# Kernel optimization log

Hardware: AMD Instinct MI355X
Metric: run time of the kernel (lower is better)

Reference implementation:

```python
import jax, jax.numpy as jnp
import numpy as np

B, N, F_IN, H, C = 256, 512, 14, 30, 2
CLUSTERS = [8, 4, 2, 1]


def _gcn(x, adj, W, b):
    # DenseGCNConv: set diagonal of adj to 1 (self loops), sym-normalize, propagate
    n = adj.shape[-1]
    eye = jnp.eye(n, dtype=adj.dtype)
    a = adj * (1.0 - eye) + eye
    dis = jnp.clip(a.sum(-1), 1.0, None) ** -0.5  # [B, n]
    a = dis[..., :, None] * a * dis[..., None, :]
    return jnp.einsum('bij,bjh->bih', a, x @ W) + b


def _diff_pool(x, adj, W, b):
    # DiffPool module applies softmax over node dim (dim=1), then
    # dense_diff_pool applies softmax over cluster dim (dim=-1)
    s = jax.nn.softmax(x @ W + b, axis=1)
    s = jax.nn.softmax(s, axis=-1)          # [B, n, c]
    xp = jnp.einsum('bnc,bnf->bcf', s, x)
    ap = jnp.einsum('bnc,bnm,bmd->bcd', s, adj, s)
    link = jnp.linalg.norm(adj - jnp.einsum('bnc,bmc->bnm', s, s)) / adj.size
    ent = jnp.mean(jnp.sum(-s * jnp.log(s + 1e-15), axis=-1))
    return xp, ap, link, ent


def _forward(x, adj, cws, cbs, pws, pbs, lw, lb):
    r = jax.nn.relu
    x = r(_gcn(x, adj, cws[0], cbs[0]))
    x = r(_gcn(x, adj, cws[1], cbs[1]))
    x = r(_gcn(x, adj, cws[2], cbs[2]))
    x = _gcn(x, adj, cws[3], cbs[3])        # no relu before first pool
    x, adj, _, _ = _diff_pool(x, adj, pws[0], pbs[0])
    x = r(_gcn(x, adj, cws[4], cbs[4]))
    x, adj, _, _ = _diff_pool(x, adj, pws[1], pbs[1])
    x = r(_gcn(x, adj, cws[5], cbs[5]))
    x, adj, _, _ = _diff_pool(x, adj, pws[2], pbs[2])
    x = r(_gcn(x, adj, cws[6], cbs[6]))
    x, adj, _, _ = _diff_pool(x, adj, pws[3], pbs[3])
    x = r(_gcn(x, adj, cws[7], cbs[7]))     # [B, 1, H]
    return (x @ lw + lb).squeeze()          # [B, C]


def setup_inputs() -> dict:
    key = jax.random.key(0)
    ks = jax.random.split(key, 40)
    inp = {}
    inp['x'] = jax.random.normal(ks[0], (B, N, F_IN), jnp.float32)
    inp['adj'] = (jax.random.uniform(ks[1], (B, N, N)) < 0.05).astype(jnp.float32)
    inp['edge_index'] = jax.random.randint(ks[2], (2, 4096), 0, N, dtype=jnp.int32)
    inp['batch'] = jnp.zeros((B * N,), jnp.int32)
    dims = [(F_IN, H)] + [(H, H)] * 7
    for i, (di, do) in enumerate(dims):
        inp[f'cw{i}'] = jax.random.normal(ks[3 + i], (di, do), jnp.float32) * (di ** -0.5)
        inp[f'cb{i}'] = jnp.zeros((do,), jnp.float32)
    for i, c in enumerate(CLUSTERS):
        inp[f'pw{i}'] = jax.random.normal(ks[12 + i], (H, c), jnp.float32) * (H ** -0.5)
        inp[f'pb{i}'] = jnp.zeros((c,), jnp.float32)
    inp['lw'] = jax.random.normal(ks[20], (H, C), jnp.float32) * (H ** -0.5)
    inp['lb'] = jnp.zeros((C,), jnp.float32)
    return inp


def reference(x, adj, edge_index, batch,
              cw0, cb0, cw1, cb1, cw2, cb2, cw3, cb3,
              cw4, cb4, cw5, cb5, cw6, cb6, cw7, cb7,
              pw0, pb0, pw1, pb1, pw2, pb2, pw3, pb3,
              lw, lb):
    cws = [cw0, cw1, cw2, cw3, cw4, cw5, cw6, cw7]
    cbs = [cb0, cb1, cb2, cb3, cb4, cb5, cb6, cb7]
    pws = [pw0, pw1, pw2, pw3]
    pbs = [pb0, pb1, pb2, pb3]
    return _forward(x, adj, cws, cbs, pws, pbs, lw, lb)
```

## Files before the change

kernel.cpp:

```cpp
#include <hip/hip_runtime.h>
#include <cstdint>
#include <cstddef>

#define B_ 256
#define N_ 512
#define RCAP 72
#define STRX 36

typedef unsigned short u16;

constexpr size_t O_COLIDX = 0;
constexpr size_t O_ROWCNT = 18874368;
constexpr size_t O_DIS    = 19398656;
constexpr size_t O_DIAG   = 19922944;

__global__ __launch_bounds__(256) void build_sparse(
    const float* __restrict__ adj, u16* __restrict__ colidx,
    int* __restrict__ rowcnt, float* __restrict__ dis, float* __restrict__ diagv)
{
    int row  = blockIdx.x * 4 + (threadIdx.x >> 6);
    int lane = threadIdx.x & 63;
    int i    = row & (N_ - 1);
    const float4* arow = (const float4*)(adj + (size_t)row * N_);
    float4 v0 = arow[lane];
    float4 v1 = arow[lane + 64];
    float vals[8] = {v0.x, v0.y, v0.z, v0.w, v1.x, v1.y, v1.z, v1.w};

    float sum = 0.f, dloc = 0.f;
    int cnt = 0;
    #pragma unroll
    for (int k = 0; k < 8; ++k) {
        int jc = (k < 4) ? (lane * 4 + k) : (256 + lane * 4 + (k - 4));
        float v = vals[k];
        if (jc == i) dloc = v;
        else { sum += v; if (v != 0.f) ++cnt; }
    }
    int pre = cnt;
    #pragma unroll
    for (int d = 1; d < 64; d <<= 1) { int y = __shfl_up(pre, d, 64); if (lane >= d) pre += y; }
    int excl  = pre - cnt;
    int total = __shfl(pre, 63, 64);
    #pragma unroll
    for (int d = 32; d > 0; d >>= 1) { sum += __shfl_xor(sum, d, 64); dloc += __shfl_xor(dloc, d, 64); }

    u16* cb = colidx + (size_t)row * RCAP;
    int c2 = 0;
    #pragma unroll
    for (int k = 0; k < 8; ++k) {
        int jc = (k < 4) ? (lane * 4 + k) : (256 + lane * 4 + (k - 4));
        float v = vals[k];
        if (jc != i && v != 0.f) { int p = excl + c2; if (p < RCAP) cb[p] = (u16)jc; ++c2; }
    }
    int base = total > RCAP ? RCAP : total;
    int p1 = base + lane;      if (p1 < RCAP) cb[p1] = (u16)N_;
    int p2 = base + 64 + lane; if (p2 < RCAP) cb[p2] = (u16)N_;
    if (lane == 0) {
        rowcnt[row] = (base + 7) >> 3;
        dis[row]    = rsqrtf(fmaxf(1.f, sum + 1.f));
        diagv[row]  = dloc;
    }
}

template <int FIN, bool RELU>
__device__ __forceinline__ void gcn_layer(
    int t, float di, int nch, const u16* __restrict__ CIDX, float* __restrict__ XA,
    const float* __restrict__ Wg, const float* __restrict__ bg, float* xr)
{
    float acc[32];
    #pragma unroll
    for (int h = 0; h < 32; ++h) acc[h] = 0.f;
    #pragma unroll
    for (int f = 0; f < FIN; ++f) {
        float xv = xr[f];
        #pragma unroll
        for (int h = 0; h < 30; ++h) acc[h] = fmaf(xv, Wg[f * 30 + h], acc[h]);
    }
    #pragma unroll
    for (int h = 0; h < 30; ++h) acc[h] *= di;
    #pragma unroll
    for (int d = 0; d < 8; ++d)
        *(float4*)&XA[t * STRX + 4 * d] =
            make_float4(acc[4*d], acc[4*d+1], acc[4*d+2], acc[4*d+3]);
    __syncthreads();

    for (int ch = 0; ch < nch; ++ch) {
        uint4 cw = *(const uint4*)&CIDX[t * RCAP + ch * 8];
        int j0 = (int)(cw.x & 0xffffu), j1 = (int)(cw.x >> 16);
        int j2 = (int)(cw.y & 0xffffu), j3 = (int)(cw.y >> 16);
        int j4 = (int)(cw.z & 0xffffu), j5 = (int)(cw.z >> 16);
        int j6 = (int)(cw.w & 0xffffu), j7 = (int)(cw.w >> 16);
        #define ACCROW(JJ) { const float* rp = &XA[(JJ) * STRX]; \
            _Pragma("unroll") for (int d = 0; d < 8; ++d) { \
                const float4 v = *(const float4*)&rp[4 * d]; \
                acc[4*d+0] += v.x; acc[4*d+1] += v.y; \
                acc[4*d+2] += v.z; acc[4*d+3] += v.w; } }
        ACCROW(j0) ACCROW(j1) ACCROW(j2) ACCROW(j3)
        ACCROW(j4) ACCROW(j5) ACCROW(j6) ACCROW(j7)
        #undef ACCROW
    }
    #pragma unroll
    for (int h = 0; h < 30; ++h) {
        float r = fmaf(di, acc[h], bg[h]);
        if (RELU) r = fmaxf(r, 0.f);
        xr[h] = r;
    }
    __syncthreads();
}

__device__ void gcn_small(int n, int t, const float* X, float* XN, float* XW, float* DIS,
                          const float* A, const float* W, const float* Bias, bool relu)
{
    if (t < n) {
        float s = 1.f;
        for (int jj = 0; jj < n; ++jj) if (jj != t) s += A[t * 8 + jj];
        DIS[t] = rsqrtf(fmaxf(1.f, s));
    }
    __syncthreads();
    if (t < n * 30) {
        int i = t / 30, h = t - i * 30;
        float acc = 0.f;
        #pragma unroll
        for (int f = 0; f < 30; ++f) acc += X[i * 30 + f] * W[f * 30 + h];
        XW[t] = acc * DIS[i];
    }
    __syncthreads();
    if (t < n * 30) {
        int i = t / 30, h = t - i * 30;
        float acc = XW[i * 30 + h];
        for (int jj = 0; jj < n; ++jj) if (jj != i) acc += A[i * 8 + jj] * XW[jj * 30 + h];
        float r = DIS[i] * acc + Bias[h];
        if (relu) r = fmaxf(r, 0.f);
        XN[t] = r;
    }
    __syncthreads();
}

__device__ void pool_small(int n, int c, int t, const float* X, const float* A,
                           const float* PW, const float* PB,
                           float* S, float* T, float* LG, float* XN, float* AN)
{
    if (t < n * c) {
        int i = t / c, k = t - i * c;
        float acc = PB[k];
        #pragma unroll
        for (int h = 0; h < 30; ++h) acc += X[i * 30 + h] * PW[h * c + k];
        LG[i * 8 + k] = acc;
    }
    __syncthreads();
    if (t < c) {
        float mx = -1e30f;
        for (int i = 0; i < n; ++i) mx = fmaxf(mx, LG[i * 8 + t]);
        float sm = 0.f;
        for (int i = 0; i < n; ++i) { float e = __expf(LG[i * 8 + t] - mx); LG[i * 8 + t] = e; sm += e; }
        float inv = 1.f / sm;
        for (int i = 0; i < n; ++i) LG[i * 8 + t] *= inv;
    }
    __syncthreads();
    if (t < n) {
        float mx = -1e30f;
        for (int k = 0; k < c; ++k) mx = fmaxf(mx, LG[t * 8 + k]);
        float sm = 0.f;
        for (int k = 0; k < c; ++k) { float e = __expf(LG[t * 8 + k] - mx); S[t * 8 + k] = e; sm += e; }
        float inv = 1.f / sm;
        for (int k = 0; k < c; ++k) S[t * 8 + k] *= inv;
    }
    __syncthreads();
    if (t < c * 30) {
        int k = t / 30, f = t - k * 30;
        float acc = 0.f;
        for (int i = 0; i < n; ++i) acc += S[i * 8 + k] * X[i * 30 + f];
        XN[t] = acc;
    }
    if (t < n * c) {
        int i = t / c, d = t - i * c;
        float acc = 0.f;
        for (int m = 0; m < n; ++m) acc += A[i * 8 + m] * S[m * 8 + d];
        T[i * 8 + d] = acc;
    }
    __syncthreads();
    if (t < c * c) {
        int k = t / c, d = t - k * c;
        float acc = 0.f;
        for (int i = 0; i < n; ++i) acc += S[i * 8 + k] * T[i * 8 + d];
        AN[k * 8 + d] = acc;
    }
    __syncthreads();
}

__global__ __launch_bounds__(512) void mega2_kernel(
    const float* __restrict__ x0,
    const float* __restrict__ W0, const float* __restrict__ Bs0,
    const float* __restrict__ W1, const float* __restrict__ Bs1,
    const float* __restrict__ W2, const float* __restrict__ Bs2,
    const float* __restrict__ W3, const float* __restrict__ Bs3,
    const float* __restrict__ pw, const float* __restrict__ pb,
    const float* cw4, const float* cb4, const float* cw5, const float* cb5,
    const float* cw6, const float* cb6, const float* cw7, const float* cb7,
    const float* pw1, const float* pb1, const float* pw2, const float* pb2,
    const float* pw3, const float* pb3, const float* lw, const float* lb,
    const u16* __restrict__ colidx, const int* __restrict__ rowcnt,
    const float* __restrict__ dis, const float* __restrict__ diagv,
    float* __restrict__ out)
{
    __shared__ __align__(16) u16   CIDX[N_ * RCAP];
    __shared__ __align__(16) float XA[(N_ + 1) * STRX];
    __shared__ float bufX[240], bufY[240], TXW[240], TDIS[8];
    __shared__ float bufA[64], bufB[64], TS[64], TT[64], TLG[64];

    const int b = blockIdx.x, t = threadIdx.x;

    {
        const unsigned* g32 = (const unsigned*)(colidx + (size_t)b * N_ * RCAP);
        unsigned* l32 = (unsigned*)CIDX;
        #pragma unroll
        for (int i = 0; i < N_ * RCAP / 2; i += 512) l32[i + t] = g32[i + t];
    }
    int   nch = rowcnt[(size_t)b * N_ + t];
    float di  = dis  [(size_t)b * N_ + t];
    float dg  = diagv[(size_t)b * N_ + t];

    if (t < STRX) XA[N_ * STRX + t] = 0.f;

    float xr[30];
    {
        const float2* xrow = (const float2*)(x0 + ((size_t)b * N_ + t) * 14);
        #pragma unroll
        for (int k = 0; k < 7; ++k) { float2 v = xrow[k]; xr[2*k] = v.x; xr[2*k+1] = v.y; }
    }
    __syncthreads();

    gcn_layer<14, true >(t, di, nch, CIDX, XA, W0, Bs0, xr);
    gcn_layer<30, true >(t, di, nch, CIDX, XA, W1, Bs1, xr);
    gcn_layer<30, true >(t, di, nch, CIDX, XA, W2, Bs2, xr);
    gcn_layer<30, false>(t, di, nch, CIDX, XA, W3, Bs3, xr);

    float* ls   = XA;
    float* ltp  = XA + 6156;
    float* red  = XA + 12300;
    float* red2 = XA + 14348;
    float* X3   = (float*)CIDX;

    {
        float lg[8];
        #pragma unroll
        for (int c = 0; c < 8; ++c) lg[c] = pb[c];
        #pragma unroll
        for (int h = 0; h < 30; ++h) {
            float xv = xr[h];
            #pragma unroll
            for (int c = 0; c < 8; ++c) lg[c] = fmaf(xv, pw[h * 8 + c], lg[c]);
        }
        *(float4*)&ls[t * 12]     = make_float4(lg[0], lg[1], lg[2], lg[3]);
        *(float4*)&ls[t * 12 + 4] = make_float4(lg[4], lg[5], lg[6], lg[7]);
        if (t < 8) ls[N_ * 12 + t] = 0.f;
    }
    __syncthreads();
    {
        int c = t >> 6, lane = t & 63;
        float v[8]; float mx = -1e30f;
        #pragma unroll
        for (int k = 0; k < 8; ++k) { v[k] = ls[(k * 64 + lane) * 12 + c]; mx = fmaxf(mx, v[k]); }
        #pragma unroll
        for (int d = 32; d > 0; d >>= 1) mx = fmaxf(mx, __shfl_xor(mx, d, 64));
        float sm = 0.f;
        #pragma unroll
        for (int k = 0; k < 8; ++k) { v[k] = __expf(v[k] - mx); sm += v[k]; }
        #pragma unroll
        for (int d = 32; d > 0; d >>= 1) sm += __shfl_xor(sm, d, 64);
        float inv = 1.f / sm;
        #pragma unroll
        for (int k = 0; k < 8; ++k) ls[(k * 64 + lane) * 12 + c] = v[k] * inv;
    }
    __syncthreads();
    float s8[8];
    {
        float mx = -1e30f;
        #pragma unroll
        for (int c = 0; c < 8; ++c) { s8[c] = ls[t * 12 + c]; mx = fmaxf(mx, s8[c]); }
        float sm = 0.f;
        #pragma unroll
        for (int c = 0; c < 8; ++c) { s8[c] = __expf(s8[c] - mx); sm += s8[c]; }
        float inv = 1.f / sm;
        #pragma unroll
        for (int c = 0; c < 8; ++c) s8[c] *= inv;
        *(float4*)&ls[t * 12]     = make_float4(s8[0], s8[1], s8[2], s8[3]);
        *(float4*)&ls[t * 12 + 4] = make_float4(s8[4], s8[5], s8[6], s8[7]);
    }
    __syncthreads();
    {
        float a8[8];
        #pragma unroll
        for (int d = 0; d < 8; ++d) a8[d] = dg * s8[d];
        for (int ch = 0; ch < nch; ++ch) {
            uint4 cw = *(const uint4*)&CIDX[t * RCAP + ch * 8];
            #define LTROW(JJ) { const float4 u0 = *(const float4*)&ls[(JJ) * 12]; \
                                const float4 u1 = *(const float4*)&ls[(JJ) * 12 + 4]; \
                                a8[0]+=u0.x; a8[1]+=u0.y; a8[2]+=u0.z; a8[3]+=u0.w; \
                                a8[4]+=u1.x; a8[5]+=u1.y; a8[6]+=u1.z; a8[7]+=u1.w; }
            LTROW((int)(cw.x & 0xffffu)) LTROW((int)(cw.x >> 16))
            LTROW((int)(cw.y & 0xffffu)) LTROW((int)(cw.y >> 16))
            LTROW((int)(cw.z & 0xffffu)) LTROW((int)(cw.z >> 16))
            LTROW((int)(cw.w & 0xffffu)) LTROW((int)(cw.w >> 16))
            #undef LTROW
        }
        __syncthreads();
        *(float4*)&ltp[t * 12]     = make_float4(a8[0], a8[1], a8[2], a8[3]);
        *(float4*)&ltp[t * 12 + 4] = make_float4(a8[4], a8[5], a8[6], a8[7]);
    }
    #pragma unroll
    for (int d = 0; d < 7; ++d)
        *(float4*)&X3[t * STRX + 4 * d] =
            make_float4(xr[4*d], xr[4*d+1], xr[4*d+2], xr[4*d+3]);
    *(float4*)&X3[t * STRX + 28] = make_float4(xr[28], xr[29], 0.f, 0.f);
    __syncthreads();
    {
        int seg = t >> 6, cd = t & 63, c = cd >> 3, dd = cd & 7;
        float a0 = 0.f, a1 = 0.f, a2 = 0.f, a3 = 0.f;
        for (int n = seg * 64; n < seg * 64 + 64; ++n) {
            float sv = ls[n * 12 + c];
            const float4 xv = *(const float4*)&X3[n * STRX + 4 * dd];
            a0 = fmaf(sv, xv.x, a0); a1 = fmaf(sv, xv.y, a1);
            a2 = fmaf(sv, xv.z, a2); a3 = fmaf(sv, xv.w, a3);
        }
        *(float4*)&red[t * 4] = make_float4(a0, a1, a2, a3);
    }
    {
        int seg = t >> 6, c = (t >> 3) & 7, d = t & 7;
        float s1 = 0.f;
        for (int n = seg * 64; n < seg * 64 + 64; ++n)
            s1 = fmaf(ls[n * 12 + c], ltp[n * 12 + d], s1);
        red2[t] = s1;
    }
    __syncthreads();
    if (t < 240) {
        int c = t / 30, f = t - c * 30, dd = f >> 2, m = f & 3;
        float s1 = 0.f;
        #pragma unroll
        for (int seg = 0; seg < 8; ++seg) s1 += red[(seg * 64 + c * 8 + dd) * 4 + m];
        bufX[t] = s1;
    }
    if (t < 64) {
        float s1 = 0.f;
        #pragma unroll
        for (int k = 0; k < 8; ++k) s1 += red2[k * 64 + t];
        bufA[t] = s1;
    }
    __syncthreads();

    float *X = bufX, *XN = bufY, *A = bufA, *AN = bufB;
    gcn_small(8, t, X, XN, TXW, TDIS, A, cw4, cb4, true);    { float* tm = X; X = XN; XN = tm; }
    pool_small(8, 4, t, X, A, pw1, pb1, TS, TT, TLG, XN, AN); { float* tm = X; X = XN; XN = tm; tm = A; A = AN; AN = tm; }
    gcn_small(4, t, X, XN, TXW, TDIS, A, cw5, cb5, true);    { float* tm = X; X = XN; XN = tm; }
    pool_small(4, 2, t, X, A, pw2, pb2, TS, TT, TLG, XN, AN); { float* tm = X; X = XN; XN = tm; tm = A; A = AN; AN = tm; }
    gcn_small(2, t, X, XN, TXW, TDIS, A, cw6, cb6, true);    { float* tm = X; X = XN; XN = tm; }
    pool_small(2, 1, t, X, A, pw3, pb3, TS, TT, TLG, XN, AN); { float* tm = X; X = XN; XN = tm; tm = A; A = AN; AN = tm; }
    gcn_small(1, t, X, XN, TXW, TDIS, A, cw7, cb7, true);    { float* tm = X; X = XN; XN = tm; }

    if (t < 2) {
        float acc = lb[t];
        #pragma unroll
        for (int h = 0; h < 30; ++h) acc += X[h] * lw[h * 2 + t];
        out[(size_t)b * 2 + t] = acc;
    }
}

extern "C" void kernel_launch(void* const* d_in, const int* in_sizes, int n_in,
                              void* d_out, int out_size, void* d_ws, size_t ws_size,
                              hipStream_t stream)
{
    const float* x   = (const float*)d_in[0];
    const float* adj = (const float*)d_in[1];
    const float *cw[8], *cb[8], *pw[4], *pb[4];
    for (int i = 0; i < 8; ++i) { cw[i] = (const float*)d_in[4 + 2 * i]; cb[i] = (const float*)d_in[5 + 2 * i]; }
    for (int i = 0; i < 4; ++i) { pw[i] = (const float*)d_in[20 + 2 * i]; pb[i] = (const float*)d_in[21 + 2 * i]; }
    const float* lw = (const float*)d_in[28];
    const float* lb = (const float*)d_in[29];

    char* ws = (char*)d_ws;
    u16*   colidx = (u16*)(ws + O_COLIDX);
    int*   rowcnt = (int*)(ws + O_ROWCNT);
    float* dis0   = (float*)(ws + O_DIS);
    float* diag0  = (float*)(ws + O_DIAG);

    build_sparse<<<(B_ * N_) / 4, 256, 0, stream>>>(adj, colidx, rowcnt, dis0, diag0);
    mega2_kernel<<<B_, 512, 0, stream>>>(x,
        cw[0], cb[0], cw[1], cb[1], cw[2], cb[2], cw[3], cb[3],
        pw[0], pb[0],
        cw[4], cb[4], cw[5], cb[5], cw[6], cb[6], cw[7], cb[7],
        pw[1], pb[1], pw[2], pb[2], pw[3], pb[3], lw, lb,
        colidx, rowcnt, dis0, diag0, (float*)d_out);
}
```

Measured before the change: 173.7 us.

## Split GCN feature dimension across two thread halves with 1024-thread blocks

Doubles the block to 1024 threads so each node is handled by two threads, each owning half of the 30 hidden features (16 and 14). This halves per-thread accumulation registers and work in the sparse aggregation and the pooling phases. Because the shared-memory scratch for the final node features no longer fits, those features are spilled to a global workspace buffer and read back for the pooled-feature reduction. The cost is extra barriers and exchanges to rebuild full rows between layers, plus the global round trip.

```diff
diff --git a/kernel.cpp b/kernel.cpp
--- a/kernel.cpp
+++ b/kernel.cpp
@@ -13,6 +13,7 @@
 constexpr size_t O_ROWCNT = 18874368;
 constexpr size_t O_DIS    = 19398656;
 constexpr size_t O_DIAG   = 19922944;
+constexpr size_t O_X3G    = 20447232;
 
 __global__ __launch_bounds__(256) void build_sparse(
     const float* __restrict__ adj, u16* __restrict__ colidx,
@@ -62,35 +63,46 @@
 }
 
 template <int FIN, bool RELU>
-__device__ __forceinline__ void gcn_layer(
-    int t, float di, int nch, const u16* __restrict__ CIDX, float* __restrict__ XA,
-    const float* __restrict__ Wg, const float* __restrict__ bg, float* xr)
-{
-    float acc[32];
-    #pragma unroll
-    for (int h = 0; h < 32; ++h) acc[h] = 0.f;
-    #pragma unroll
-    for (int f = 0; f < FIN; ++f) {
-        float xv = xr[f];
-        #pragma unroll
-        for (int h = 0; h < 30; ++h) acc[h] = fmaf(xv, Wg[f * 30 + h], acc[h]);
-    }
-    #pragma unroll
-    for (int h = 0; h < 30; ++h) acc[h] *= di;
-    #pragma unroll
-    for (int d = 0; d < 8; ++d)
-        *(float4*)&XA[t * STRX + 4 * d] =
+__device__ __forceinline__ void glayer(
+    int n, int hf, float di, int nch, const u16* __restrict__ CIDX,
+    float* __restrict__ XA, const float* __restrict__ W,
+    const float* __restrict__ Bs, float* xr)
+{
+    float acc[16];
+    #pragma unroll
+    for (int h = 0; h < 16; ++h) acc[h] = 0.f;
+    if (hf == 0) {
+        #pragma unroll
+        for (int f = 0; f < FIN; ++f) {
+            float xv = xr[f];
+            #pragma unroll
+            for (int h = 0; h < 16; ++h) acc[h] = fmaf(xv, W[f * 30 + h], acc[h]);
+        }
+    } else {
+        #pragma unroll
+        for (int f = 0; f < FIN; ++f) {
+            float xv = xr[f];
+            #pragma unroll
+            for (int h = 0; h < 14; ++h) acc[h] = fmaf(xv, W[f * 30 + 16 + h], acc[h]);
+        }
+    }
+    #pragma unroll
+    for (int h = 0; h < 16; ++h) acc[h] *= di;
+    int ho = hf * 16;
+    #pragma unroll
+    for (int d = 0; d < 4; ++d)
+        *(float4*)&XA[n * STRX + ho + 4 * d] =
             make_float4(acc[4*d], acc[4*d+1], acc[4*d+2], acc[4*d+3]);
     __syncthreads();
 
     for (int ch = 0; ch < nch; ++ch) {
-        uint4 cw = *(const uint4*)&CIDX[t * RCAP + ch * 8];
+        uint4 cw = *(const uint4*)&CIDX[n * RCAP + ch * 8];
         int j0 = (int)(cw.x & 0xffffu), j1 = (int)(cw.x >> 16);
         int j2 = (int)(cw.y & 0xffffu), j3 = (int)(cw.y >> 16);
         int j4 = (int)(cw.z & 0xffffu), j5 = (int)(cw.z >> 16);
         int j6 = (int)(cw.w & 0xffffu), j7 = (int)(cw.w >> 16);
-        #define ACCROW(JJ) { const float* rp = &XA[(JJ) * STRX]; \
-            _Pragma("unroll") for (int d = 0; d < 8; ++d) { \
+        #define ACCROW(JJ) { const float* rp = &XA[(JJ) * STRX + ho]; \
+            _Pragma("unroll") for (int d = 0; d < 4; ++d) { \
                 const float4 v = *(const float4*)&rp[4 * d]; \
                 acc[4*d+0] += v.x; acc[4*d+1] += v.y; \
                 acc[4*d+2] += v.z; acc[4*d+3] += v.w; } }
@@ -98,11 +110,44 @@
         ACCROW(j4) ACCROW(j5) ACCROW(j6) ACCROW(j7)
         #undef ACCROW
     }
-    #pragma unroll
-    for (int h = 0; h < 30; ++h) {
-        float r = fmaf(di, acc[h], bg[h]);
-        if (RELU) r = fmaxf(r, 0.f);
-        xr[h] = r;
+    float rr[16];
+    if (hf == 0) {
+        #pragma unroll
+        for (int h = 0; h < 16; ++h) {
+            float r = fmaf(di, acc[h], Bs[h]);
+            rr[h] = RELU ? fmaxf(r, 0.f) : r;
+        }
+    } else {
+        #pragma unroll
+        for (int h = 0; h < 14; ++h) {
+            float r = fmaf(di, acc[h], Bs[16 + h]);
+            rr[h] = RELU ? fmaxf(r, 0.f) : r;
+        }
+        rr[14] = 0.f; rr[15] = 0.f;
+    }
+    __syncthreads();
+    #pragma unroll
+    for (int d = 0; d < 4; ++d)
+        *(float4*)&XA[n * STRX + ho + 4 * d] =
+            make_float4(rr[4*d], rr[4*d+1], rr[4*d+2], rr[4*d+3]);
+    __syncthreads();
+    if (hf == 0) {
+        #pragma unroll
+        for (int h = 0; h < 16; ++h) xr[h] = rr[h];
+        #pragma unroll
+        for (int d = 0; d < 4; ++d) {
+            const float4 v = *(const float4*)&XA[n * STRX + 16 + 4 * d];
+            if (d < 3) { xr[16+4*d] = v.x; xr[17+4*d] = v.y; xr[18+4*d] = v.z; xr[19+4*d] = v.w; }
+            else       { xr[28] = v.x; xr[29] = v.y; }
+        }
+    } else {
+        #pragma unroll
+        for (int h = 0; h < 14; ++h) xr[16 + h] = rr[h];
+        #pragma unroll
+        for (int d = 0; d < 4; ++d) {
+            const float4 v = *(const float4*)&XA[n * STRX + 4 * d];
+            xr[4*d] = v.x; xr[4*d+1] = v.y; xr[4*d+2] = v.z; xr[4*d+3] = v.w;
+        }
     }
     __syncthreads();
 }
@@ -187,7 +232,7 @@
     __syncthreads();
 }
 
-__global__ __launch_bounds__(512) void mega2_kernel(
+__global__ __launch_bounds__(1024) void mega3_kernel(
     const float* __restrict__ x0,
     const float* __restrict__ W0, const float* __restrict__ Bs0,
     const float* __restrict__ W1, const float* __restrict__ Bs1,
@@ -200,7 +245,7 @@
     const float* pw3, const float* pb3, const float* lw, const float* lb,
     const u16* __restrict__ colidx, const int* __restrict__ rowcnt,
     const float* __restrict__ dis, const float* __restrict__ diagv,
-    float* __restrict__ out)
+    float* __restrict__ x3g, float* __restrict__ out)
 {
     __shared__ __align__(16) u16   CIDX[N_ * RCAP];
     __shared__ __align__(16) float XA[(N_ + 1) * STRX];
@@ -208,54 +253,64 @@
     __shared__ float bufA[64], bufB[64], TS[64], TT[64], TLG[64];
 
     const int b = blockIdx.x, t = threadIdx.x;
+    const int n = t & (N_ - 1), hf = t >> 9;
 
     {
         const unsigned* g32 = (const unsigned*)(colidx + (size_t)b * N_ * RCAP);
         unsigned* l32 = (unsigned*)CIDX;
         #pragma unroll
-        for (int i = 0; i < N_ * RCAP / 2; i += 512) l32[i + t] = g32[i + t];
-    }
-    int   nch = rowcnt[(size_t)b * N_ + t];
-    float di  = dis  [(size_t)b * N_ + t];
-    float dg  = diagv[(size_t)b * N_ + t];
-
+        for (int i = 0; i < N_ * RCAP / 2; i += 1024) l32[i + t] = g32[i + t];
+    }
+    int   nch = rowcnt[(size_t)b * N_ + n];
+    float di  = dis  [(size_t)b * N_ + n];
+    float dg  = diagv[(size_t)b * N_ + n];
     if (t < STRX) XA[N_ * STRX + t] = 0.f;
 
     float xr[30];
     {
-        const float2* xrow = (const float2*)(x0 + ((size_t)b * N_ + t) * 14);
+        const float2* xrow = (const float2*)(x0 + ((size_t)b * N_ + n) * 14);
         #pragma unroll
         for (int k = 0; k < 7; ++k) { float2 v = xrow[k]; xr[2*k] = v.x; xr[2*k+1] = v.y; }
     }
     __syncthreads();
 
-    gcn_layer<14, true >(t, di, nch, CIDX, XA, W0, Bs0, xr);
-    gcn_layer<30, true >(t, di, nch, CIDX, XA, W1, Bs1, xr);
-    gcn_layer<30, true >(t, di, nch, CIDX, XA, W2, Bs2, xr);
-    gcn_layer<30, false>(t, di, nch, CIDX, XA, W3, Bs3, xr);
+    glayer<14, true >(n, hf, di, nch, CIDX, XA, W0, Bs0, xr);
+    glayer<30, true >(n, hf, di, nch, CIDX, XA, W1, Bs1, xr);
+    glayer<30, true >(n, hf, di, nch, CIDX, XA, W2, Bs2, xr);
+    glayer<30, false>(n, hf, di, nch, CIDX, XA, W3, Bs3, xr);
+
+    {
+        float4* xgw = (float4*)(x3g + (size_t)b * N_ * 32);
+        #pragma unroll
+        for (int i = 0; i < 4; ++i) {
+            int e4 = t + i * 1024;
+            int nn = e4 >> 3, q = e4 & 7;
+            xgw[e4] = *(const float4*)&XA[nn * STRX + 4 * q];
+        }
+    }
+    float lg[4];
+    {
+        int c0 = hf * 4;
+        #pragma unroll
+        for (int c = 0; c < 4; ++c) lg[c] = pb[c0 + c];
+        #pragma unroll
+        for (int h = 0; h < 30; ++h) {
+            float xv = xr[h];
+            #pragma unroll
+            for (int c = 0; c < 4; ++c) lg[c] = fmaf(xv, pw[h * 8 + c0 + c], lg[c]);
+        }
+    }
+    __syncthreads();
 
     float* ls   = XA;
     float* ltp  = XA + 6156;
     float* red  = XA + 12300;
-    float* red2 = XA + 14348;
-    float* X3   = (float*)CIDX;
-
-    {
-        float lg[8];
-        #pragma unroll
-        for (int c = 0; c < 8; ++c) lg[c] = pb[c];
-        #pragma unroll
-        for (int h = 0; h < 30; ++h) {
-            float xv = xr[h];
-            #pragma unroll
-            for (int c = 0; c < 8; ++c) lg[c] = fmaf(xv, pw[h * 8 + c], lg[c]);
-        }
-        *(float4*)&ls[t * 12]     = make_float4(lg[0], lg[1], lg[2], lg[3]);
-        *(float4*)&ls[t * 12 + 4] = make_float4(lg[4], lg[5], lg[6], lg[7]);
-        if (t < 8) ls[N_ * 12 + t] = 0.f;
-    }
-    __syncthreads();
-    {
+    float* red2 = XA + 16396;
+
+    *(float4*)&ls[n * 12 + hf * 4] = make_float4(lg[0], lg[1], lg[2], lg[3]);
+    if (t < 12) ls[N_ * 12 + t] = 0.f;
+    __syncthreads();
+    if (t < 512) {
         int c = t >> 6, lane = t & 63;
         float v[8]; float mx = -1e30f;
         #pragma unroll
@@ -272,53 +327,42 @@
         for (int k = 0; k < 8; ++k) ls[(k * 64 + lane) * 12 + c] = v[k] * inv;
     }
     __syncthreads();
-    float s8[8];
-    {
-        float mx = -1e30f;
-        #pragma unroll
-        for (int c = 0; c < 8; ++c) { s8[c] = ls[t * 12 + c]; mx = fmaxf(mx, s8[c]); }
+    if (t < 512) {
+        float v[8]; float mx = -1e30f;
+        #pragma unroll
+        for (int c = 0; c < 8; ++c) { v[c] = ls[t * 12 + c]; mx = fmaxf(mx, v[c]); }
         float sm = 0.f;
         #pragma unroll
-        for (int c = 0; c < 8; ++c) { s8[c] = __expf(s8[c] - mx); sm += s8[c]; }
+        for (int c = 0; c < 8; ++c) { v[c] = __expf(v[c] - mx); sm += v[c]; }
         float inv = 1.f / sm;
-        #pragma unroll
-        for (int c = 0; c < 8; ++c) s8[c] *= inv;
-        *(float4*)&ls[t * 12]     = make_float4(s8[0], s8[1], s8[2], s8[3]);
-        *(float4*)&ls[t * 12 + 4] = make_float4(s8[4], s8[5], s8[6], s8[7]);
-    }
-    __syncthreads();
-    {
-        float a8[8];
-        #pragma unroll
-        for (int d = 0; d < 8; ++d) a8[d] = dg * s8[d];
+        *(float4*)&ls[t * 12]     = make_float4(v[0]*inv, v[1]*inv, v[2]*inv, v[3]*inv);
+        *(float4*)&ls[t * 12 + 4] = make_float4(v[4]*inv, v[5]*inv, v[6]*inv, v[7]*inv);
+    }
+    __syncthreads();
+    {
+        int d0 = hf * 4;
+        const float4 sown = *(const float4*)&ls[n * 12 + d0];
+        float a0 = dg * sown.x, a1 = dg * sown.y, a2 = dg * sown.z, a3 = dg * sown.w;
         for (int ch = 0; ch < nch; ++ch) {
-            uint4 cw = *(const uint4*)&CIDX[t * RCAP + ch * 8];
-            #define LTROW(JJ) { const float4 u0 = *(const float4*)&ls[(JJ) * 12]; \
-                                const float4 u1 = *(const float4*)&ls[(JJ) * 12 + 4]; \
-                                a8[0]+=u0.x; a8[1]+=u0.y; a8[2]+=u0.z; a8[3]+=u0.w; \
-                                a8[4]+=u1.x; a8[5]+=u1.y; a8[6]+=u1.z; a8[7]+=u1.w; }
+            uint4 cw = *(const uint4*)&CIDX[n * RCAP + ch * 8];
+            #define LTROW(JJ) { const float4 u0 = *(const float4*)&ls[(JJ) * 12 + d0]; \
+                                a0 += u0.x; a1 += u0.y; a2 += u0.z; a3 += u0.w; }
             LTROW((int)(cw.x & 0xffffu)) LTROW((int)(cw.x >> 16))
             LTROW((int)(cw.y & 0xffffu)) LTROW((int)(cw.y >> 16))
             LTROW((int)(cw.z & 0xffffu)) LTROW((int)(cw.z >> 16))
             LTROW((int)(cw.w & 0xffffu)) LTROW((int)(cw.w >> 16))
             #undef LTROW
         }
-        __syncthreads();
-        *(float4*)&ltp[t * 12]     = make_float4(a8[0], a8[1], a8[2], a8[3]);
-        *(float4*)&ltp[t * 12 + 4] = make_float4(a8[4], a8[5], a8[6], a8[7]);
-    }
-    #pragma unroll
-    for (int d = 0; d < 7; ++d)
-        *(float4*)&X3[t * STRX + 4 * d] =
-            make_float4(xr[4*d], xr[4*d+1], xr[4*d+2], xr[4*d+3]);
-    *(float4*)&X3[t * STRX + 28] = make_float4(xr[28], xr[29], 0.f, 0.f);
+        *(float4*)&ltp[n * 12 + d0] = make_float4(a0, a1, a2, a3);
+    }
     __syncthreads();
     {
         int seg = t >> 6, cd = t & 63, c = cd >> 3, dd = cd & 7;
+        const float4* xg = (const float4*)(x3g + (size_t)b * N_ * 32);
         float a0 = 0.f, a1 = 0.f, a2 = 0.f, a3 = 0.f;
-        for (int n = seg * 64; n < seg * 64 + 64; ++n) {
-            float sv = ls[n * 12 + c];
-            const float4 xv = *(const float4*)&X3[n * STRX + 4 * dd];
+        for (int nn = seg * 32; nn < seg * 32 + 32; ++nn) {
+            float sv = ls[nn * 12 + c];
+            const float4 xv = xg[nn * 8 + dd];
             a0 = fmaf(sv, xv.x, a0); a1 = fmaf(sv, xv.y, a1);
             a2 = fmaf(sv, xv.z, a2); a3 = fmaf(sv, xv.w, a3);
         }
@@ -327,8 +371,8 @@
     {
         int seg = t >> 6, c = (t >> 3) & 7, d = t & 7;
         float s1 = 0.f;
-        for (int n = seg * 64; n < seg * 64 + 64; ++n)
-            s1 = fmaf(ls[n * 12 + c], ltp[n * 12 + d], s1);
+        for (int nn = seg * 32; nn < seg * 32 + 32; ++nn)
+            s1 = fmaf(ls[nn * 12 + c], ltp[nn * 12 + d], s1);
         red2[t] = s1;
     }
     __syncthreads();
@@ -336,14 +380,14 @@
         int c = t / 30, f = t - c * 30, dd = f >> 2, m = f & 3;
         float s1 = 0.f;
         #pragma unroll
-        for (int seg = 0; seg < 8; ++seg) s1 += red[(seg * 64 + c * 8 + dd) * 4 + m];
+        for (int seg = 0; seg < 16; ++seg) s1 += red[(seg * 64 + c * 8 + dd) * 4 + m];
         bufX[t] = s1;
-    }
-    if (t < 64) {
+    } else if (t >= 256 && t < 320) {
+        int tt = t - 256;
         float s1 = 0.f;
         #pragma unroll
-        for (int k = 0; k < 8; ++k) s1 += red2[k * 64 + t];
-        bufA[t] = s1;
+        for (int seg = 0; seg < 16; ++seg) s1 += red2[seg * 64 + tt];
+        bufA[tt] = s1;
     }
     __syncthreads();
 
@@ -381,12 +425,13 @@
     int*   rowcnt = (int*)(ws + O_ROWCNT);
     float* dis0   = (float*)(ws + O_DIS);
     float* diag0  = (float*)(ws + O_DIAG);
+    float* x3g    = (float*)(ws + O_X3G);
 
     build_sparse<<<(B_ * N_) / 4, 256, 0, stream>>>(adj, colidx, rowcnt, dis0, diag0);
-    mega2_kernel<<<B_, 512, 0, stream>>>(x,
+    mega3_kernel<<<B_, 1024, 0, stream>>>(x,
         cw[0], cb[0], cw[1], cb[1], cw[2], cb[2], cw[3], cb[3],
         pw[0], pb[0],
         cw[4], cb[4], cw[5], cb[5], cw[6], cb[6], cw[7], cb[7],
         pw[1], pb[1], pw[2], pb[2], pw[3], pb[3], lw, lb,
-        colidx, rowcnt, dis0, diag0, (float*)d_out);
-}
+        colidx, rowcnt, dis0, diag0, x3g, (float*)d_out);
+}
```

Result: faster. 144.5 us (median of 2 runs) (-16.8%).
